# Kernel optimization log

Measured on AMD Instinct MI355X. Metric: run time of the kernel, lower is better.

The kernel has to match this reference:

```python
import jax, jax.numpy as jnp
import numpy as np

# Llama config (TinyLlama-scale)
L, H, KVH, D = 2, 32, 8, 64      # layers, q heads, kv heads, head_dim
DM, FF, V = 2048, 8192, 32000    # d_model, intermediate, vocab
B, S = 1, 1024                   # batch, seq_len
EPS, THETA = 1e-5, 10000.0


def setup_inputs() -> dict:
    key = jax.random.key(0)
    ks = jax.random.split(key, 10)
    w = lambda k, shape: jax.random.normal(k, shape, jnp.float32) * 0.02
    return {
        "input_ids": jax.random.randint(ks[0], (B, S), 0, V, dtype=jnp.int32),
        "embed": w(ks[1], (V, DM)),
        "wq": w(ks[2], (L, DM, H * D)),
        "wk": w(ks[3], (L, DM, KVH * D)),
        "wv": w(ks[4], (L, DM, KVH * D)),
        "wo": w(ks[5], (L, H * D, DM)),
        "wgate": w(ks[6], (L, DM, FF)),
        "wup": w(ks[7], (L, DM, FF)),
        "wdown": w(ks[8], (L, FF, DM)),
        "ln1": jnp.ones((L, DM), jnp.float32),
        "ln2": jnp.ones((L, DM), jnp.float32),
    }


def _rms(h, g):
    return h * jax.lax.rsqrt(jnp.mean(h * h, axis=-1, keepdims=True) + EPS) * g


def _rotate_half(t):
    t1, t2 = jnp.split(t, 2, axis=-1)
    return jnp.concatenate([-t2, t1], axis=-1)


def reference(input_ids, embed, wq, wk, wv, wo, wgate, wup, wdown, ln1, ln2):
    x = embed[input_ids]                                  # (B,S,DM)
    # rotary embeddings (HF llama style)
    inv_freq = 1.0 / (THETA ** (jnp.arange(0, D, 2, dtype=jnp.float32) / D))
    freqs = jnp.arange(S, dtype=jnp.float32)[:, None] * inv_freq[None, :]
    emb = jnp.concatenate([freqs, freqs], axis=-1)        # (S,D)
    cos = jnp.cos(emb)[None, None]                        # (1,1,S,D)
    sin = jnp.sin(emb)[None, None]
    # eager causal additive mask (1,1,S,S)
    mask = jnp.triu(jnp.full((1, 1, S, S), jnp.finfo(jnp.float32).min, jnp.float32), k=1)
    scale = 1.0 / np.sqrt(D).astype(np.float32)
    for l in range(L):
        # self-attention block
        h = _rms(x, ln1[l])
        q = (h @ wq[l]).reshape(B, S, H, D).transpose(0, 2, 1, 3)     # (B,H,S,D)
        k = (h @ wk[l]).reshape(B, S, KVH, D).transpose(0, 2, 1, 3)   # (B,KVH,S,D)
        v = (h @ wv[l]).reshape(B, S, KVH, D).transpose(0, 2, 1, 3)
        q = q * cos + _rotate_half(q) * sin
        k = k * cos + _rotate_half(k) * sin
        k = jnp.repeat(k, H // KVH, axis=1)                           # GQA expand
        v = jnp.repeat(v, H // KVH, axis=1)
        scores = jnp.einsum('bhqd,bhkd->bhqk', q, k) * scale + mask   # eager path
        probs = jax.nn.softmax(scores, axis=-1)
        attn = jnp.einsum('bhqk,bhkd->bhqd', probs, v)
        attn = attn.transpose(0, 2, 1, 3).reshape(B, S, H * D)
        x = x + attn @ wo[l]
        # SwiGLU MLP block
        h = _rms(x, ln2[l])
        x = x + (jax.nn.silu(h @ wgate[l]) * (h @ wup[l])) @ wdown[l]
    return x
```

## Files before the change

kernel.cpp:

```cpp
#include <hip/hip_runtime.h>
#include <hip/hip_bf16.h>
#include <math.h>

#define NL 2
#define NH 32
#define NKVH 8
#define HD 64
#define DM 2048
#define FF 8192
#define SEQ 1024
#define QKVW 3072
#define RMS_EPS 1e-5f

typedef short s8v __attribute__((ext_vector_type(8)));
typedef short s4v __attribute__((ext_vector_type(4)));
typedef float f32x4 __attribute__((ext_vector_type(4)));
typedef __hip_bfloat16 bf16;

__global__ __launch_bounds__(256) void embed_kernel(const int* __restrict__ ids,
                                                    const float* __restrict__ emb,
                                                    float* __restrict__ x) {
    int s = blockIdx.x;
    int row = ids[s];
    const float4* src = (const float4*)(emb + (size_t)row * DM);
    float4* dst = (float4*)(x + (size_t)s * DM);
    #pragma unroll
    for (int i = 0; i < 2; ++i)
        dst[threadIdx.x + i * 256] = src[threadIdx.x + i * 256];
}

__global__ __launch_bounds__(256) void rms_kernel(const float* __restrict__ x,
                                                  const float* __restrict__ g,
                                                  bf16* __restrict__ out) {
    int s = blockIdx.x;
    const float4* row = (const float4*)(x + (size_t)s * DM);
    float4 v0 = row[threadIdx.x * 2];
    float4 v1 = row[threadIdx.x * 2 + 1];
    float ss = v0.x*v0.x + v0.y*v0.y + v0.z*v0.z + v0.w*v0.w
             + v1.x*v1.x + v1.y*v1.y + v1.z*v1.z + v1.w*v1.w;
    #pragma unroll
    for (int o = 32; o > 0; o >>= 1) ss += __shfl_down(ss, o, 64);
    __shared__ float red[4];
    if ((threadIdx.x & 63) == 0) red[threadIdx.x >> 6] = ss;
    __syncthreads();
    float total = red[0] + red[1] + red[2] + red[3];
    float inv = 1.0f / sqrtf(total / (float)DM + RMS_EPS);
    const float4* g4 = (const float4*)g;
    float4 ga = g4[threadIdx.x * 2], gb = g4[threadIdx.x * 2 + 1];
    union { bf16 h[8]; s8v v; } u;
    u.h[0] = __float2bfloat16(v0.x * inv * ga.x);
    u.h[1] = __float2bfloat16(v0.y * inv * ga.y);
    u.h[2] = __float2bfloat16(v0.z * inv * ga.z);
    u.h[3] = __float2bfloat16(v0.w * inv * ga.w);
    u.h[4] = __float2bfloat16(v1.x * inv * gb.x);
    u.h[5] = __float2bfloat16(v1.y * inv * gb.y);
    u.h[6] = __float2bfloat16(v1.z * inv * gb.z);
    u.h[7] = __float2bfloat16(v1.w * inv * gb.w);
    *(s8v*)(out + (size_t)s * DM + threadIdx.x * 8) = u.v;
}

template<bool OUTBF>
__global__ __launch_bounds__(256) void gemm_f32w_kernel(const bf16* __restrict__ A, int Ka,
                                                        const float* __restrict__ Wa, int Na,
                                                        const float* __restrict__ Wb, int Nb,
                                                        const float* __restrict__ Wc,
                                                        float* __restrict__ C,
                                                        bf16* __restrict__ Cb,
                                                        int M, int N, int Kchunk) {
    __shared__ bf16 As[2][128 * 64];
    __shared__ bf16 Bs[2][128 * 64];
    const int t = threadIdx.x, lane = t & 63;
    const int w = t >> 6;
    const int m0 = blockIdx.y * 128, n0 = blockIdx.x * 128;
    const size_t koff = (size_t)blockIdx.z * Kchunk;

    const int nl = t & 127;
    const int kob = t >> 7;
    const int ng = n0 + nl;
    const float* wp; int wstr;
    if (ng < Na)           { wp = Wa + ng;             wstr = Na; }
    else if (ng < Na + Nb) { wp = Wb + (ng - Na);      wstr = Nb; }
    else                   { wp = Wc + (ng - Na - Nb); wstr = N - Na - Nb; }
    wp += koff * (size_t)wstr;

    const int ako = t & 7, am = t >> 3;
    const bf16* apt = A + (size_t)(m0 + am) * Ka + koff + ako * 8;

    const int wm = (w >> 1) * 64, wn = (w & 1) * 64;
    const int fr = lane & 15, sl = lane >> 4;

    f32x4 acc[4][4];
    f32x4 z = {0.f, 0.f, 0.f, 0.f};
    #pragma unroll
    for (int i = 0; i < 4; ++i)
        #pragma unroll
        for (int j = 0; j < 4; ++j) acc[i][j] = z;

    float rb[4][8];
    s8v ra[4];

    auto LOADR = [&](int tile) {
        const int k0 = tile * 64;
        #pragma unroll
        for (int u = 0; u < 4; ++u) {
            const float* p = wp + (size_t)(k0 + (kob + 2 * u) * 8) * wstr;
            #pragma unroll
            for (int j = 0; j < 8; ++j) rb[u][j] = p[(size_t)j * wstr];
            ra[u] = *(const s8v*)(apt + (size_t)(32 * u) * Ka + k0);
        }
    };
    auto WRITE = [&](bf16* AsB, bf16* BsB) {
        #pragma unroll
        for (int u = 0; u < 4; ++u) {
            union { bf16 h[8]; s8v v; } cv;
            #pragma unroll
            for (int j = 0; j < 8; ++j) cv.h[j] = __float2bfloat16(rb[u][j]);
            int ko = kob + 2 * u;
            *(s8v*)((char*)BsB + nl * 128 + ((ko * 16) ^ ((nl & 7) << 4))) = cv.v;
            int m = am + 32 * u;
            *(s8v*)((char*)AsB + m * 128 + ((ako * 16) ^ ((m & 7) << 4))) = ra[u];
        }
    };
    auto COMPUTE = [&](const bf16* AsB, const bf16* BsB) {
        #pragma unroll
        for (int kk = 0; kk < 2; ++kk) {
            const int kb = kk * 64 + sl * 16;
            s8v af[4], bfv[4];
            #pragma unroll
            for (int i = 0; i < 4; ++i) {
                int m = wm + i * 16 + fr;
                af[i] = *(const s8v*)((const char*)AsB + m * 128 + (kb ^ ((m & 7) << 4)));
            }
            #pragma unroll
            for (int j = 0; j < 4; ++j) {
                int n = wn + j * 16 + fr;
                bfv[j] = *(const s8v*)((const char*)BsB + n * 128 + (kb ^ ((n & 7) << 4)));
            }
            #pragma unroll
            for (int i = 0; i < 4; ++i)
                #pragma unroll
                for (int j = 0; j < 4; ++j)
                    acc[i][j] = __builtin_amdgcn_mfma_f32_16x16x32_bf16(af[i], bfv[j], acc[i][j], 0, 0, 0);
        }
    };

    const int nt = Kchunk / 64;
    LOADR(0);
    WRITE(&As[0][0], &Bs[0][0]);
    __syncthreads();
    for (int tt = 0; tt < nt; ++tt) {
        const int cur = tt & 1;
        if (tt + 1 < nt) LOADR(tt + 1);
        COMPUTE(&As[cur][0], &Bs[cur][0]);
        if (tt + 1 < nt) {
            __syncthreads();
            WRITE(&As[cur ^ 1][0], &Bs[cur ^ 1][0]);
            __syncthreads();
        }
    }

    float* Cz = C + (size_t)blockIdx.z * M * N;
    #pragma unroll
    for (int i = 0; i < 4; ++i) {
        #pragma unroll
        for (int j = 0; j < 4; ++j) {
            #pragma unroll
            for (int q = 0; q < 4; ++q) {
                int row = m0 + wm + i * 16 + sl * 4 + q;
                int col = n0 + wn + j * 16 + fr;
                float vv = acc[i][j][q];
                if constexpr (OUTBF) Cb[(size_t)row * N + col] = __float2bfloat16(vv);
                else                 Cz[(size_t)row * N + col] = vv;
            }
        }
    }
}

__global__ __launch_bounds__(512) void gemm256_kernel(const bf16* __restrict__ A, int Ka,
                                                      const float* __restrict__ Wa, int Na,
                                                      const float* __restrict__ Wb,
                                                      bf16* __restrict__ Cb,
                                                      int M, int N, int K) {
    __shared__ bf16 As[2][256 * 64];
    __shared__ bf16 Bs[2][256 * 64];
    const int t = threadIdx.x, lane = t & 63;
    const int w = t >> 6;
    const int m0 = blockIdx.y * 256, n0 = blockIdx.x * 256;

    const int nl = t & 255;
    const int kob = t >> 8;
    const int ng = n0 + nl;
    const float* wp; int wstr;
    if (ng < Na) { wp = Wa + ng;        wstr = Na; }
    else         { wp = Wb + (ng - Na); wstr = N - Na; }

    const int ako = t & 7, am = t >> 3;
    const bf16* apt = A + (size_t)(m0 + am) * Ka + ako * 8;

    const int wm = (w >> 2) * 128, wn = (w & 3) * 64;
    const int fr = lane & 15, sl = lane >> 4;

    f32x4 acc[8][4];
    f32x4 z = {0.f, 0.f, 0.f, 0.f};
    #pragma unroll
    for (int i = 0; i < 8; ++i)
        #pragma unroll
        for (int j = 0; j < 4; ++j) acc[i][j] = z;

    float rb[4][8];
    s8v ra[4];

    auto LOADR = [&](int tile) {
        const int k0 = tile * 64;
        #pragma unroll
        for (int u = 0; u < 4; ++u) {
            const float* p = wp + (size_t)(k0 + (kob + 2 * u) * 8) * wstr;
            #pragma unroll
            for (int j = 0; j < 8; ++j) rb[u][j] = p[(size_t)j * wstr];
            ra[u] = *(const s8v*)(apt + (size_t)(64 * u) * Ka + k0);
        }
    };
    auto WRITE = [&](bf16* AsB, bf16* BsB) {
        #pragma unroll
        for (int u = 0; u < 4; ++u) {
            union { bf16 h[8]; s8v v; } cv;
            #pragma unroll
            for (int j = 0; j < 8; ++j) cv.h[j] = __float2bfloat16(rb[u][j]);
            int ko = kob + 2 * u;
            *(s8v*)((char*)BsB + nl * 128 + ((ko * 16) ^ ((nl & 7) << 4))) = cv.v;
            int m = am + 64 * u;
            *(s8v*)((char*)AsB + m * 128 + ((ako * 16) ^ ((m & 7) << 4))) = ra[u];
        }
    };
    auto COMPUTE = [&](const bf16* AsB, const bf16* BsB) {
        #pragma unroll
        for (int kk = 0; kk < 2; ++kk) {
            const int kb = kk * 64 + sl * 16;
            s8v af[8], bfv[4];
            #pragma unroll
            for (int i = 0; i < 8; ++i) {
                int m = wm + i * 16 + fr;
                af[i] = *(const s8v*)((const char*)AsB + m * 128 + (kb ^ ((m & 7) << 4)));
            }
            #pragma unroll
            for (int j = 0; j < 4; ++j) {
                int n = wn + j * 16 + fr;
                bfv[j] = *(const s8v*)((const char*)BsB + n * 128 + (kb ^ ((n & 7) << 4)));
            }
            #pragma unroll
            for (int i = 0; i < 8; ++i)
                #pragma unroll
                for (int j = 0; j < 4; ++j)
                    acc[i][j] = __builtin_amdgcn_mfma_f32_16x16x32_bf16(af[i], bfv[j], acc[i][j], 0, 0, 0);
        }
    };

    const int nt = K / 64;
    LOADR(0);
    WRITE(&As[0][0], &Bs[0][0]);
    __syncthreads();
    for (int tt = 0; tt < nt; ++tt) {
        const int cur = tt & 1;
        if (tt + 1 < nt) LOADR(tt + 1);
        COMPUTE(&As[cur][0], &Bs[cur][0]);
        if (tt + 1 < nt) {
            __syncthreads();
            WRITE(&As[cur ^ 1][0], &Bs[cur ^ 1][0]);
            __syncthreads();
        }
    }

    #pragma unroll
    for (int i = 0; i < 8; ++i) {
        #pragma unroll
        for (int j = 0; j < 4; ++j) {
            #pragma unroll
            for (int q = 0; q < 4; ++q) {
                int row = m0 + wm + i * 16 + sl * 4 + q;
                int col = n0 + wn + j * 16 + fr;
                Cb[(size_t)row * N + col] = __float2bfloat16(acc[i][j][q]);
            }
        }
    }
}

__global__ __launch_bounds__(256) void reduce4_kernel(float* __restrict__ x,
                                                      const float* __restrict__ p) {
    const int n4 = SEQ * DM / 4;
    int i = blockIdx.x * 256 + threadIdx.x;
    if (i >= n4) return;
    float4 a = ((const float4*)x)[i];
    #pragma unroll
    for (int c = 0; c < 4; ++c) {
        float4 v = ((const float4*)p)[i + c * n4];
        a.x += v.x; a.y += v.y; a.z += v.z; a.w += v.w;
    }
    ((float4*)x)[i] = a;
}

__global__ __launch_bounds__(256) void rope_qk_kernel(const float* __restrict__ qkv,
                                                      bf16* __restrict__ Qh,
                                                      bf16* __restrict__ Kh) {
    int idx = blockIdx.x * 256 + threadIdx.x;
    int i = idx & 31;
    int hh = (idx >> 5) % (NH + NKVH);
    int s = idx / (32 * (NH + NKVH));
    bool isq = hh < NH;
    int col = isq ? hh * HD + i : DM + (hh - NH) * HD + i;
    float a = qkv[(size_t)s * QKVW + col];
    float b = qkv[(size_t)s * QKVW + col + 32];
    float inv = exp2f(-(float)i * 0.41524101186092029f);
    float ang = (float)s * inv;
    float c = cosf(ang), sn = sinf(ang);
    float ra = a * c - b * sn;
    float rb = b * c + a * sn;
    if (isq) {
        bf16* p = Qh + ((size_t)hh * SEQ + s) * HD + i;
        p[0]  = __float2bfloat16(ra);
        p[32] = __float2bfloat16(rb);
    } else {
        bf16* p = Kh + ((size_t)(hh - NH) * SEQ + s) * HD + i;
        p[0]  = __float2bfloat16(ra);
        p[32] = __float2bfloat16(rb);
    }
}

__global__ __launch_bounds__(256) void vtrans_kernel(const float* __restrict__ qkv,
                                                     bf16* __restrict__ Vt) {
    __shared__ float tile[64][65];
    const int s0 = blockIdx.x * 64;
    const int kvh = blockIdx.y;
    const int tx = threadIdx.x & 63, ty = threadIdx.x >> 6;
    #pragma unroll
    for (int i = 0; i < 16; ++i)
        tile[i * 4 + ty][tx] = qkv[(size_t)(s0 + i * 4 + ty) * QKVW + DM + 512 + kvh * HD + tx];
    __syncthreads();
    #pragma unroll
    for (int i = 0; i < 16; ++i) {
        int d = i * 4 + ty;
        Vt[((size_t)kvh * HD + d) * SEQ + s0 + tx] = __float2bfloat16(tile[tx][d]);
    }
}

__global__ __launch_bounds__(256) void attn_mfma_kernel(const bf16* __restrict__ Qh,
                                                        const bf16* __restrict__ Kh,
                                                        const bf16* __restrict__ Vt,
                                                        bf16* __restrict__ o) {
    __shared__ char lds[32768];
    char* Qs = lds;
    char* Ks = lds + 8192;
    char* Vs = lds + 16384;
    char* Ps = lds + 24576;
    const int t = threadIdx.x, lane = t & 63, w = t >> 6;
    const int g = lane >> 4, lo = lane & 15;
    const int h = blockIdx.y, kvh = h >> 2;
    const int qbase = blockIdx.x * 64;
    const int strip = w * 16;
    const bf16* qsrc = Qh + ((size_t)h * SEQ + qbase) * HD;
    const bf16* ksrc = Kh + (size_t)kvh * SEQ * HD;
    const bf16* vsrc = Vt + (size_t)kvh * HD * SEQ;

    #pragma unroll
    for (int c = t; c < 512; c += 256) {
        int row = c >> 3, col = c & 7;
        *(s8v*)(Qs + row * 128 + ((col * 16) ^ ((row & 7) << 4))) =
            *(const s8v*)(qsrc + row * HD + col * 8);
    }

    f32x4 oacc[4];
    f32x4 z = {0.f, 0.f, 0.f, 0.f};
    #pragma unroll
    for (int dj = 0; dj < 4; ++dj) oacc[dj] = z;
    float m0[4], lsum[4];
    #pragma unroll
    for (int r = 0; r < 4; ++r) { m0[r] = -INFINITY; lsum[r] = 0.f; }

    const int qt = blockIdx.x;
    for (int kt = 0; kt <= qt; ++kt) {
        __syncthreads();
        const bf16* kq = ksrc + (size_t)(kt * 64) * HD;
        const bf16* vq = vsrc + kt * 64;
        #pragma unroll
        for (int c = t; c < 512; c += 256) {
            int row = c >> 3, col = c & 7;
            int swz = (col * 16) ^ ((row & 7) << 4);
            *(s8v*)(Ks + row * 128 + swz) = *(const s8v*)(kq + row * HD + col * 8);
            *(s8v*)(Vs + row * 128 + swz) = *(const s8v*)(vq + (size_t)row * SEQ + col * 8);
        }
        __syncthreads();

        s8v qa0 = *(const s8v*)(Qs + (strip + lo) * 128 + ((g * 16) ^ ((lo & 7) << 4)));
        s8v qa1 = *(const s8v*)(Qs + (strip + lo) * 128 + ((64 + g * 16) ^ ((lo & 7) << 4)));
        f32x4 sacc[4];
        #pragma unroll
        for (int j = 0; j < 4; ++j) {
            s8v kb0 = *(const s8v*)(Ks + (j * 16 + lo) * 128 + ((g * 16) ^ ((lo & 7) << 4)));
            s8v kb1 = *(const s8v*)(Ks + (j * 16 + lo) * 128 + ((64 + g * 16) ^ ((lo & 7) << 4)));
            f32x4 sv = __builtin_amdgcn_mfma_f32_16x16x32_bf16(qa0, kb0, z, 0, 0, 0);
            sacc[j] = __builtin_amdgcn_mfma_f32_16x16x32_bf16(qa1, kb1, sv, 0, 0, 0);
        }
        #pragma unroll
        for (int j = 0; j < 4; ++j) {
            int kgl = kt * 64 + j * 16 + lo;
            #pragma unroll
            for (int r = 0; r < 4; ++r) {
                int qgl = qbase + strip + g * 4 + r;
                float sv = sacc[j][r] * 0.125f;
                sacc[j][r] = (kgl <= qgl) ? sv : -INFINITY;
            }
        }
        float rmax[4], resc[4];
        #pragma unroll
        for (int r = 0; r < 4; ++r) {
            float mx = fmaxf(fmaxf(sacc[0][r], sacc[1][r]), fmaxf(sacc[2][r], sacc[3][r]));
            mx = fmaxf(mx, __shfl_xor(mx, 1, 64));
            mx = fmaxf(mx, __shfl_xor(mx, 2, 64));
            mx = fmaxf(mx, __shfl_xor(mx, 4, 64));
            mx = fmaxf(mx, __shfl_xor(mx, 8, 64));
            float mn = fmaxf(m0[r], mx);
            resc[r] = expf(m0[r] - mn);
            m0[r] = mn;
            rmax[r] = mn;
        }
        #pragma unroll
        for (int j = 0; j < 4; ++j)
            #pragma unroll
            for (int r = 0; r < 4; ++r)
                sacc[j][r] = expf(sacc[j][r] - rmax[r]);
        #pragma unroll
        for (int r = 0; r < 4; ++r) {
            float ps = sacc[0][r] + sacc[1][r] + sacc[2][r] + sacc[3][r];
            lsum[r] = lsum[r] * resc[r] + ps;
        }
        #pragma unroll
        for (int dj = 0; dj < 4; ++dj)
            #pragma unroll
            for (int r = 0; r < 4; ++r)
                oacc[dj][r] *= resc[r];
        #pragma unroll
        for (int j = 0; j < 4; ++j) {
            #pragma unroll
            for (int r = 0; r < 4; ++r) {
                int prow = strip + g * 4 + r;
                int pcol = j * 16 + lo;
                *(bf16*)(Ps + prow * 128 + ((pcol * 2) ^ ((prow & 7) << 4))) =
                    __float2bfloat16(sacc[j][r]);
            }
        }
        s8v pa0 = *(const s8v*)(Ps + (strip + lo) * 128 + ((g * 16) ^ ((lo & 7) << 4)));
        s8v pa1 = *(const s8v*)(Ps + (strip + lo) * 128 + ((64 + g * 16) ^ ((lo & 7) << 4)));
        #pragma unroll
        for (int dj = 0; dj < 4; ++dj) {
            s8v vb0 = *(const s8v*)(Vs + (dj * 16 + lo) * 128 + ((g * 16) ^ ((lo & 7) << 4)));
            s8v vb1 = *(const s8v*)(Vs + (dj * 16 + lo) * 128 + ((64 + g * 16) ^ ((lo & 7) << 4)));
            oacc[dj] = __builtin_amdgcn_mfma_f32_16x16x32_bf16(pa0, vb0, oacc[dj], 0, 0, 0);
            oacc[dj] = __builtin_amdgcn_mfma_f32_16x16x32_bf16(pa1, vb1, oacc[dj], 0, 0, 0);
        }
    }
    float invl[4];
    #pragma unroll
    for (int r = 0; r < 4; ++r) {
        float l = lsum[r];
        l += __shfl_xor(l, 1, 64);
        l += __shfl_xor(l, 2, 64);
        l += __shfl_xor(l, 4, 64);
        l += __shfl_xor(l, 8, 64);
        invl[r] = 1.f / l;
    }
    #pragma unroll
    for (int dj = 0; dj < 4; ++dj) {
        #pragma unroll
        for (int r = 0; r < 4; ++r) {
            int qrow = qbase + strip + g * 4 + r;
            o[(size_t)qrow * DM + h * HD + dj * 16 + lo] =
                __float2bfloat16(oacc[dj][r] * invl[r]);
        }
    }
}

__global__ __launch_bounds__(256) void silu_mul_kernel(const bf16* __restrict__ gu,
                                                       bf16* __restrict__ ga) {
    int i = blockIdx.x * 256 + threadIdx.x;
    int s = i >> 10;
    int c8 = i & 1023;
    union { s8v v; bf16 h[8]; } gv, uv, ov;
    gv.v = *(const s8v*)(gu + (size_t)s * (2 * FF) + c8 * 8);
    uv.v = *(const s8v*)(gu + (size_t)s * (2 * FF) + FF + c8 * 8);
    #pragma unroll
    for (int j = 0; j < 8; ++j) {
        float g = __bfloat162float(gv.h[j]);
        float u = __bfloat162float(uv.h[j]);
        ov.h[j] = __float2bfloat16(g / (1.f + expf(-g)) * u);
    }
    *(s8v*)(ga + (size_t)s * FF + c8 * 8) = ov.v;
}

extern "C" void kernel_launch(void* const* d_in, const int* in_sizes, int n_in,
                              void* d_out, int out_size, void* d_ws, size_t ws_size,
                              hipStream_t stream) {
    const int*   ids   = (const int*)d_in[0];
    const float* emb   = (const float*)d_in[1];
    const float* wq    = (const float*)d_in[2];
    const float* wk    = (const float*)d_in[3];
    const float* wv    = (const float*)d_in[4];
    const float* wo    = (const float*)d_in[5];
    const float* wgate = (const float*)d_in[6];
    const float* wup   = (const float*)d_in[7];
    const float* wdown = (const float*)d_in[8];
    const float* ln1   = (const float*)d_in[9];
    const float* ln2   = (const float*)d_in[10];
    float* x = (float*)d_out;

    bf16* h_bf  = (bf16*)d_ws;
    bf16* attnb = h_bf  + (size_t)SEQ * DM;
    bf16* gub   = attnb + (size_t)SEQ * DM;
    bf16* gab   = gub   + (size_t)SEQ * 2 * FF;
    bf16* Qhb   = gab   + (size_t)SEQ * FF;
    bf16* Khb   = Qhb   + (size_t)NH * SEQ * HD;
    bf16* Vtb   = Khb   + (size_t)NKVH * SEQ * HD;
    float* qkv  = (float*)(Vtb + (size_t)NKVH * HD * SEQ);
    float* psum = qkv + (size_t)SEQ * QKVW;

    embed_kernel<<<SEQ, 256, 0, stream>>>(ids, emb, x);

    for (int l = 0; l < NL; ++l) {
        const float* wq_l = wq + (size_t)l * DM * DM;
        const float* wk_l = wk + (size_t)l * DM * 512;
        const float* wv_l = wv + (size_t)l * DM * 512;
        const float* wo_l = wo + (size_t)l * DM * DM;
        const float* wg_l = wgate + (size_t)l * DM * FF;
        const float* wu_l = wup   + (size_t)l * DM * FF;
        const float* wd_l = wdown + (size_t)l * FF * DM;

        rms_kernel<<<SEQ, 256, 0, stream>>>(x, ln1 + (size_t)l * DM, h_bf);

        gemm_f32w_kernel<false><<<dim3(QKVW / 128, SEQ / 128, 1), 256, 0, stream>>>(
            h_bf, DM, wq_l, DM, wk_l, 512, wv_l, qkv, nullptr, SEQ, QKVW, DM);

        rope_qk_kernel<<<(SEQ * (NH + NKVH) * 32) / 256, 256, 0, stream>>>(qkv, Qhb, Khb);
        vtrans_kernel<<<dim3(SEQ / 64, NKVH), 256, 0, stream>>>(qkv, Vtb);

        attn_mfma_kernel<<<dim3(SEQ / 64, NH), 256, 0, stream>>>(Qhb, Khb, Vtb, attnb);

        gemm_f32w_kernel<false><<<dim3(DM / 128, SEQ / 128, 4), 256, 0, stream>>>(
            attnb, DM, wo_l, DM, nullptr, 0, nullptr, psum, nullptr, SEQ, DM, DM / 4);
        reduce4_kernel<<<(SEQ * DM / 4) / 256, 256, 0, stream>>>(x, psum);

        rms_kernel<<<SEQ, 256, 0, stream>>>(x, ln2 + (size_t)l * DM, h_bf);

        gemm256_kernel<<<dim3((2 * FF) / 256, SEQ / 256), 512, 0, stream>>>(
            h_bf, DM, wg_l, FF, wu_l, gub, SEQ, 2 * FF, DM);

        silu_mul_kernel<<<(SEQ * FF / 8) / 256, 256, 0, stream>>>(gub, gab);

        gemm_f32w_kernel<false><<<dim3(DM / 128, SEQ / 128, 4), 256, 0, stream>>>(
            gab, FF, wd_l, DM, nullptr, 0, nullptr, psum, nullptr, SEQ, DM, FF / 4);
        reduce4_kernel<<<(SEQ * DM / 4) / 256, 256, 0, stream>>>(x, psum);
    }
}
```

Baseline: 624.2 us.

## Fuse RoPE and V-transpose into QKV GEMM epilogue; fuse SiLU-mul into gate/up GEMM

A dedicated QKV GEMM now applies rotary embedding to Q/K and writes transposed bf16 V directly from registers, which drops the fp32 qkv buffer and the rope and vtrans kernels. The gate/up GEMM interleaves matching gate and up column tiles per block, passes the up half through LDS and applies SiLU*up in the epilogue, which drops the intermediate gu buffer and the silu kernel. The aim is to save launches and global round trips. The cost is scattered bf16 stores and cos/sin evaluation in the epilogue, plus a 128KB LDS footprint in the gate/up kernel.

After: 722.3 us. +15.7%, slower.

```diff
diff --git a/kernel.cpp b/kernel.cpp
--- a/kernel.cpp
+++ b/kernel.cpp
@@ -59,13 +59,9 @@
     *(s8v*)(out + (size_t)s * DM + threadIdx.x * 8) = u.v;
 }
 
-template<bool OUTBF>
 __global__ __launch_bounds__(256) void gemm_f32w_kernel(const bf16* __restrict__ A, int Ka,
                                                         const float* __restrict__ Wa, int Na,
-                                                        const float* __restrict__ Wb, int Nb,
-                                                        const float* __restrict__ Wc,
                                                         float* __restrict__ C,
-                                                        bf16* __restrict__ Cb,
                                                         int M, int N, int Kchunk) {
     __shared__ bf16 As[2][128 * 64];
     __shared__ bf16 Bs[2][128 * 64];
@@ -76,12 +72,8 @@
 
     const int nl = t & 127;
     const int kob = t >> 7;
-    const int ng = n0 + nl;
-    const float* wp; int wstr;
-    if (ng < Na)           { wp = Wa + ng;             wstr = Na; }
-    else if (ng < Na + Nb) { wp = Wb + (ng - Na);      wstr = Nb; }
-    else                   { wp = Wc + (ng - Na - Nb); wstr = N - Na - Nb; }
-    wp += koff * (size_t)wstr;
+    const float* wp = Wa + n0 + nl + koff * (size_t)Na;
+    const int wstr = Na;
 
     const int ako = t & 7, am = t >> 3;
     const bf16* apt = A + (size_t)(m0 + am) * Ka + koff + ako * 8;
@@ -168,42 +160,43 @@
             for (int q = 0; q < 4; ++q) {
                 int row = m0 + wm + i * 16 + sl * 4 + q;
                 int col = n0 + wn + j * 16 + fr;
-                float vv = acc[i][j][q];
-                if constexpr (OUTBF) Cb[(size_t)row * N + col] = __float2bfloat16(vv);
-                else                 Cz[(size_t)row * N + col] = vv;
-            }
-        }
-    }
-}
-
-__global__ __launch_bounds__(512) void gemm256_kernel(const bf16* __restrict__ A, int Ka,
-                                                      const float* __restrict__ Wa, int Na,
-                                                      const float* __restrict__ Wb,
-                                                      bf16* __restrict__ Cb,
-                                                      int M, int N, int K) {
-    __shared__ bf16 As[2][256 * 64];
-    __shared__ bf16 Bs[2][256 * 64];
+                Cz[(size_t)row * N + col] = acc[i][j][q];
+            }
+        }
+    }
+}
+
+__global__ __launch_bounds__(256) void gemm_qkv_kernel(const bf16* __restrict__ A,
+                                                       const float* __restrict__ Wq,
+                                                       const float* __restrict__ Wk,
+                                                       const float* __restrict__ Wv,
+                                                       bf16* __restrict__ Qh,
+                                                       bf16* __restrict__ Kh,
+                                                       bf16* __restrict__ Vt) {
+    __shared__ bf16 As[2][128 * 64];
+    __shared__ bf16 Bs[2][128 * 64];
     const int t = threadIdx.x, lane = t & 63;
     const int w = t >> 6;
-    const int m0 = blockIdx.y * 256, n0 = blockIdx.x * 256;
-
-    const int nl = t & 255;
-    const int kob = t >> 8;
+    const int m0 = blockIdx.y * 128, n0 = blockIdx.x * 128;
+
+    const int nl = t & 127;
+    const int kob = t >> 7;
     const int ng = n0 + nl;
     const float* wp; int wstr;
-    if (ng < Na) { wp = Wa + ng;        wstr = Na; }
-    else         { wp = Wb + (ng - Na); wstr = N - Na; }
+    if (ng < DM)            { wp = Wq + ng;          wstr = DM;  }
+    else if (ng < DM + 512) { wp = Wk + (ng - DM);   wstr = 512; }
+    else                    { wp = Wv + (ng - 2560); wstr = 512; }
 
     const int ako = t & 7, am = t >> 3;
-    const bf16* apt = A + (size_t)(m0 + am) * Ka + ako * 8;
-
-    const int wm = (w >> 2) * 128, wn = (w & 3) * 64;
+    const bf16* apt = A + (size_t)(m0 + am) * DM + ako * 8;
+
+    const int wm = (w >> 1) * 64, wn = (w & 1) * 64;
     const int fr = lane & 15, sl = lane >> 4;
 
-    f32x4 acc[8][4];
+    f32x4 acc[4][4];
     f32x4 z = {0.f, 0.f, 0.f, 0.f};
     #pragma unroll
-    for (int i = 0; i < 8; ++i)
+    for (int i = 0; i < 4; ++i)
         #pragma unroll
         for (int j = 0; j < 4; ++j) acc[i][j] = z;
 
@@ -217,7 +210,7 @@
             const float* p = wp + (size_t)(k0 + (kob + 2 * u) * 8) * wstr;
             #pragma unroll
             for (int j = 0; j < 8; ++j) rb[u][j] = p[(size_t)j * wstr];
-            ra[u] = *(const s8v*)(apt + (size_t)(64 * u) * Ka + k0);
+            ra[u] = *(const s8v*)(apt + (size_t)(32 * u) * DM + k0);
         }
     };
     auto WRITE = [&](bf16* AsB, bf16* BsB) {
@@ -228,7 +221,7 @@
             for (int j = 0; j < 8; ++j) cv.h[j] = __float2bfloat16(rb[u][j]);
             int ko = kob + 2 * u;
             *(s8v*)((char*)BsB + nl * 128 + ((ko * 16) ^ ((nl & 7) << 4))) = cv.v;
-            int m = am + 64 * u;
+            int m = am + 32 * u;
             *(s8v*)((char*)AsB + m * 128 + ((ako * 16) ^ ((m & 7) << 4))) = ra[u];
         }
     };
@@ -236,9 +229,9 @@
         #pragma unroll
         for (int kk = 0; kk < 2; ++kk) {
             const int kb = kk * 64 + sl * 16;
-            s8v af[8], bfv[4];
-            #pragma unroll
-            for (int i = 0; i < 8; ++i) {
+            s8v af[4], bfv[4];
+            #pragma unroll
+            for (int i = 0; i < 4; ++i) {
                 int m = wm + i * 16 + fr;
                 af[i] = *(const s8v*)((const char*)AsB + m * 128 + (kb ^ ((m & 7) << 4)));
             }
@@ -248,14 +241,14 @@
                 bfv[j] = *(const s8v*)((const char*)BsB + n * 128 + (kb ^ ((n & 7) << 4)));
             }
             #pragma unroll
-            for (int i = 0; i < 8; ++i)
+            for (int i = 0; i < 4; ++i)
                 #pragma unroll
                 for (int j = 0; j < 4; ++j)
                     acc[i][j] = __builtin_amdgcn_mfma_f32_16x16x32_bf16(af[i], bfv[j], acc[i][j], 0, 0, 0);
         }
     };
 
-    const int nt = K / 64;
+    const int nt = DM / 64;
     LOADR(0);
     WRITE(&As[0][0], &Bs[0][0]);
     __syncthreads();
@@ -271,14 +264,165 @@
     }
 
     #pragma unroll
-    for (int i = 0; i < 8; ++i) {
-        #pragma unroll
-        for (int j = 0; j < 4; ++j) {
-            #pragma unroll
-            for (int q = 0; q < 4; ++q) {
-                int row = m0 + wm + i * 16 + sl * 4 + q;
-                int col = n0 + wn + j * 16 + fr;
-                Cb[(size_t)row * N + col] = __float2bfloat16(acc[i][j][q]);
+    for (int j = 0; j < 4; ++j) {
+        int c = n0 + wn + j * 16 + fr;
+        if (c < 2560) {
+            if (j < 2) {
+                int ii = (wn + j * 16 + fr) & 63;
+                bf16* dst = (c < DM) ? Qh + ((size_t)(c >> 6) * SEQ) * HD
+                                     : Kh + ((size_t)((c - DM) >> 6) * SEQ) * HD;
+                float invf = exp2f(-(float)ii * 0.41524101186092029f);
+                #pragma unroll
+                for (int i = 0; i < 4; ++i) {
+                    #pragma unroll
+                    for (int q = 0; q < 4; ++q) {
+                        int s = m0 + wm + i * 16 + sl * 4 + q;
+                        float a = acc[i][j][q], b = acc[i][j + 2][q];
+                        float ang = (float)s * invf;
+                        float cs = cosf(ang), sn = sinf(ang);
+                        bf16* p = dst + (size_t)s * HD + ii;
+                        p[0]  = __float2bfloat16(a * cs - b * sn);
+                        p[32] = __float2bfloat16(b * cs + a * sn);
+                    }
+                }
+            }
+        } else {
+            int kvh = (c - 2560) >> 6, d = (c - 2560) & 63;
+            bf16* dst = Vt + ((size_t)kvh * HD + d) * SEQ;
+            #pragma unroll
+            for (int i = 0; i < 4; ++i) {
+                #pragma unroll
+                for (int q = 0; q < 4; ++q) {
+                    int s = m0 + wm + i * 16 + sl * 4 + q;
+                    dst[s] = __float2bfloat16(acc[i][j][q]);
+                }
+            }
+        }
+    }
+}
+
+__global__ __launch_bounds__(512) void gemm_gu_kernel(const bf16* __restrict__ A,
+                                                      const float* __restrict__ Wg,
+                                                      const float* __restrict__ Wu,
+                                                      bf16* __restrict__ gab) {
+    __shared__ char lds[131072];
+    const int t = threadIdx.x, lane = t & 63;
+    const int w = t >> 6;
+    const int m0 = blockIdx.y * 256, n0g = blockIdx.x * 128;
+
+    const int nl = t & 255;
+    const int kob = t >> 8;
+    const int cl = nl & 127;
+    const float* wp = ((nl < 128) ? Wg : Wu) + n0g + cl;
+    const int wstr = FF;
+
+    const int ako = t & 7, am = t >> 3;
+    const bf16* apt = A + (size_t)(m0 + am) * DM + ako * 8;
+
+    const int wm = (w >> 2) * 128, wn = (w & 3) * 64;
+    const int fr = lane & 15, sl = lane >> 4;
+
+    f32x4 acc[8][4];
+    f32x4 z = {0.f, 0.f, 0.f, 0.f};
+    #pragma unroll
+    for (int i = 0; i < 8; ++i)
+        #pragma unroll
+        for (int j = 0; j < 4; ++j) acc[i][j] = z;
+
+    float rb[4][8];
+    s8v ra[4];
+
+    auto LOADR = [&](int tile) {
+        const int k0 = tile * 64;
+        #pragma unroll
+        for (int u = 0; u < 4; ++u) {
+            const float* p = wp + (size_t)(k0 + (kob + 2 * u) * 8) * wstr;
+            #pragma unroll
+            for (int j = 0; j < 8; ++j) rb[u][j] = p[(size_t)j * wstr];
+            ra[u] = *(const s8v*)(apt + (size_t)(64 * u) * DM + k0);
+        }
+    };
+    auto WRITE = [&](char* AsB, char* BsB) {
+        #pragma unroll
+        for (int u = 0; u < 4; ++u) {
+            union { bf16 h[8]; s8v v; } cv;
+            #pragma unroll
+            for (int j = 0; j < 8; ++j) cv.h[j] = __float2bfloat16(rb[u][j]);
+            int ko = kob + 2 * u;
+            *(s8v*)(BsB + nl * 128 + ((ko * 16) ^ ((nl & 7) << 4))) = cv.v;
+            int m = am + 64 * u;
+            *(s8v*)(AsB + m * 128 + ((ako * 16) ^ ((m & 7) << 4))) = ra[u];
+        }
+    };
+    auto COMPUTE = [&](const char* AsB, const char* BsB) {
+        #pragma unroll
+        for (int kk = 0; kk < 2; ++kk) {
+            const int kb = kk * 64 + sl * 16;
+            s8v af[8], bfv[4];
+            #pragma unroll
+            for (int i = 0; i < 8; ++i) {
+                int m = wm + i * 16 + fr;
+                af[i] = *(const s8v*)(AsB + m * 128 + (kb ^ ((m & 7) << 4)));
+            }
+            #pragma unroll
+            for (int j = 0; j < 4; ++j) {
+                int n = wn + j * 16 + fr;
+                bfv[j] = *(const s8v*)(BsB + n * 128 + (kb ^ ((n & 7) << 4)));
+            }
+            #pragma unroll
+            for (int i = 0; i < 8; ++i)
+                #pragma unroll
+                for (int j = 0; j < 4; ++j)
+                    acc[i][j] = __builtin_amdgcn_mfma_f32_16x16x32_bf16(af[i], bfv[j], acc[i][j], 0, 0, 0);
+        }
+    };
+
+    const int nt = DM / 64;
+    LOADR(0);
+    WRITE(lds, lds + 65536);
+    __syncthreads();
+    for (int tt = 0; tt < nt; ++tt) {
+        const int cur = tt & 1;
+        if (tt + 1 < nt) LOADR(tt + 1);
+        COMPUTE(lds + cur * 32768, lds + 65536 + cur * 32768);
+        if (tt + 1 < nt) {
+            __syncthreads();
+            WRITE(lds + (cur ^ 1) * 32768, lds + 65536 + (cur ^ 1) * 32768);
+            __syncthreads();
+        }
+    }
+
+    __syncthreads();
+    bf16* Ups = (bf16*)lds;
+    if (wn >= 128) {
+        #pragma unroll
+        for (int i = 0; i < 8; ++i) {
+            #pragma unroll
+            for (int j = 0; j < 4; ++j) {
+                #pragma unroll
+                for (int q = 0; q < 4; ++q) {
+                    int row = wm + i * 16 + sl * 4 + q;
+                    int col = (wn - 128) + j * 16 + fr;
+                    Ups[row * 130 + col] = __float2bfloat16(acc[i][j][q]);
+                }
+            }
+        }
+    }
+    __syncthreads();
+    if (wn < 128) {
+        #pragma unroll
+        for (int i = 0; i < 8; ++i) {
+            #pragma unroll
+            for (int j = 0; j < 4; ++j) {
+                #pragma unroll
+                for (int q = 0; q < 4; ++q) {
+                    int row = wm + i * 16 + sl * 4 + q;
+                    int col = wn + j * 16 + fr;
+                    float g = acc[i][j][q];
+                    float u = __bfloat162float(Ups[row * 130 + col]);
+                    gab[(size_t)(m0 + row) * FF + n0g + col] =
+                        __float2bfloat16(g / (1.f + expf(-g)) * u);
+                }
             }
         }
     }
@@ -296,50 +440,6 @@
         a.x += v.x; a.y += v.y; a.z += v.z; a.w += v.w;
     }
     ((float4*)x)[i] = a;
-}
-
-__global__ __launch_bounds__(256) void rope_qk_kernel(const float* __restrict__ qkv,
-                                                      bf16* __restrict__ Qh,
-                                                      bf16* __restrict__ Kh) {
-    int idx = blockIdx.x * 256 + threadIdx.x;
-    int i = idx & 31;
-    int hh = (idx >> 5) % (NH + NKVH);
-    int s = idx / (32 * (NH + NKVH));
-    bool isq = hh < NH;
-    int col = isq ? hh * HD + i : DM + (hh - NH) * HD + i;
-    float a = qkv[(size_t)s * QKVW + col];
-    float b = qkv[(size_t)s * QKVW + col + 32];
-    float inv = exp2f(-(float)i * 0.41524101186092029f);
-    float ang = (float)s * inv;
-    float c = cosf(ang), sn = sinf(ang);
-    float ra = a * c - b * sn;
-    float rb = b * c + a * sn;
-    if (isq) {
-        bf16* p = Qh + ((size_t)hh * SEQ + s) * HD + i;
-        p[0]  = __float2bfloat16(ra);
-        p[32] = __float2bfloat16(rb);
-    } else {
-        bf16* p = Kh + ((size_t)(hh - NH) * SEQ + s) * HD + i;
-        p[0]  = __float2bfloat16(ra);
-        p[32] = __float2bfloat16(rb);
-    }
-}
-
-__global__ __launch_bounds__(256) void vtrans_kernel(const float* __restrict__ qkv,
-                                                     bf16* __restrict__ Vt) {
-    __shared__ float tile[64][65];
-    const int s0 = blockIdx.x * 64;
-    const int kvh = blockIdx.y;
-    const int tx = threadIdx.x & 63, ty = threadIdx.x >> 6;
-    #pragma unroll
-    for (int i = 0; i < 16; ++i)
-        tile[i * 4 + ty][tx] = qkv[(size_t)(s0 + i * 4 + ty) * QKVW + DM + 512 + kvh * HD + tx];
-    __syncthreads();
-    #pragma unroll
-    for (int i = 0; i < 16; ++i) {
-        int d = i * 4 + ty;
-        Vt[((size_t)kvh * HD + d) * SEQ + s0 + tx] = __float2bfloat16(tile[tx][d]);
-    }
 }
 
 __global__ __launch_bounds__(256) void attn_mfma_kernel(const bf16* __restrict__ Qh,
@@ -478,23 +578,6 @@
     }
 }
 
-__global__ __launch_bounds__(256) void silu_mul_kernel(const bf16* __restrict__ gu,
-                                                       bf16* __restrict__ ga) {
-    int i = blockIdx.x * 256 + threadIdx.x;
-    int s = i >> 10;
-    int c8 = i & 1023;
-    union { s8v v; bf16 h[8]; } gv, uv, ov;
-    gv.v = *(const s8v*)(gu + (size_t)s * (2 * FF) + c8 * 8);
-    uv.v = *(const s8v*)(gu + (size_t)s * (2 * FF) + FF + c8 * 8);
-    #pragma unroll
-    for (int j = 0; j < 8; ++j) {
-        float g = __bfloat162float(gv.h[j]);
-        float u = __bfloat162float(uv.h[j]);
-        ov.h[j] = __float2bfloat16(g / (1.f + expf(-g)) * u);
-    }
-    *(s8v*)(ga + (size_t)s * FF + c8 * 8) = ov.v;
-}
-
 extern "C" void kernel_launch(void* const* d_in, const int* in_sizes, int n_in,
                               void* d_out, int out_size, void* d_ws, size_t ws_size,
                               hipStream_t stream) {
@@ -513,13 +596,11 @@
 
     bf16* h_bf  = (bf16*)d_ws;
     bf16* attnb = h_bf  + (size_t)SEQ * DM;
-    bf16* gub   = attnb + (size_t)SEQ * DM;
-    bf16* gab   = gub   + (size_t)SEQ * 2 * FF;
+    bf16* gab   = attnb + (size_t)SEQ * DM;
     bf16* Qhb   = gab   + (size_t)SEQ * FF;
     bf16* Khb   = Qhb   + (size_t)NH * SEQ * HD;
     bf16* Vtb   = Khb   + (size_t)NKVH * SEQ * HD;
-    float* qkv  = (float*)(Vtb + (size_t)NKVH * HD * SEQ);
-    float* psum = qkv + (size_t)SEQ * QKVW;
+    float* psum = (float*)(Vtb + (size_t)NKVH * HD * SEQ);
 
     embed_kernel<<<SEQ, 256, 0, stream>>>(ids, emb, x);
 
@@ -534,27 +615,22 @@
 
         rms_kernel<<<SEQ, 256, 0, stream>>>(x, ln1 + (size_t)l * DM, h_bf);
 
-        gemm_f32w_kernel<false><<<dim3(QKVW / 128, SEQ / 128, 1), 256, 0, stream>>>(
-            h_bf, DM, wq_l, DM, wk_l, 512, wv_l, qkv, nullptr, SEQ, QKVW, DM);
-
-        rope_qk_kernel<<<(SEQ * (NH + NKVH) * 32) / 256, 256, 0, stream>>>(qkv, Qhb, Khb);
-        vtrans_kernel<<<dim3(SEQ / 64, NKVH), 256, 0, stream>>>(qkv, Vtb);
+        gemm_qkv_kernel<<<dim3(QKVW / 128, SEQ / 128), 256, 0, stream>>>(
+            h_bf, wq_l, wk_l, wv_l, Qhb, Khb, Vtb);
 
         attn_mfma_kernel<<<dim3(SEQ / 64, NH), 256, 0, stream>>>(Qhb, Khb, Vtb, attnb);
 
-        gemm_f32w_kernel<false><<<dim3(DM / 128, SEQ / 128, 4), 256, 0, stream>>>(
-            attnb, DM, wo_l, DM, nullptr, 0, nullptr, psum, nullptr, SEQ, DM, DM / 4);
+        gemm_f32w_kernel<<<dim3(DM / 128, SEQ / 128, 4), 256, 0, stream>>>(
+            attnb, DM, wo_l, DM, psum, SEQ, DM, DM / 4);
         reduce4_kernel<<<(SEQ * DM / 4) / 256, 256, 0, stream>>>(x, psum);
 
         rms_kernel<<<SEQ, 256, 0, stream>>>(x, ln2 + (size_t)l * DM, h_bf);
 
-        gemm256_kernel<<<dim3((2 * FF) / 256, SEQ / 256), 512, 0, stream>>>(
-            h_bf, DM, wg_l, FF, wu_l, gub, SEQ, 2 * FF, DM);
-
-        silu_mul_kernel<<<(SEQ * FF / 8) / 256, 256, 0, stream>>>(gub, gab);
-
-        gemm_f32w_kernel<false><<<dim3(DM / 128, SEQ / 128, 4), 256, 0, stream>>>(
-            gab, FF, wd_l, DM, nullptr, 0, nullptr, psum, nullptr, SEQ, DM, FF / 4);
+        gemm_gu_kernel<<<dim3(FF / 128, SEQ / 256), 512, 0, stream>>>(
+            h_bf, wg_l, wu_l, gab);
+
+        gemm_f32w_kernel<<<dim3(DM / 128, SEQ / 128, 4), 256, 0, stream>>>(
+            gab, FF, wd_l, DM, psum, SEQ, DM, FF / 4);
         reduce4_kernel<<<(SEQ * DM / 4) / 256, 256, 0, stream>>>(x, psum);
     }
 }
```

## Prefetch fp32 weight tiles two iterations ahead in GEMM main loop

Applied to the files above, without the earlier changes.

Splits the global load of the fp32 weight (B) tile from the bf16 activation (A) tile and double-buffers the weight registers (rbA/rbB). The weight load is now issued two k-tiles ahead, while the activation load stays one tile ahead, and the loop is unrolled by two with fixed LDS buffer indices. The aim is to hide the latency of the strided, uncoalesced fp32 weight reads behind more MFMA work. It doubles the weight staging registers, which may cut occupancy or cause spills.

Result: slower. 727.0 us (+16.5%).

```diff
diff --git a/kernel.cpp b/kernel.cpp
--- a/kernel.cpp
+++ b/kernel.cpp
@@ -96,20 +96,25 @@
         #pragma unroll
         for (int j = 0; j < 4; ++j) acc[i][j] = z;
 
-    float rb[4][8];
+    float rbA[4][8], rbB[4][8];
     s8v ra[4];
 
-    auto LOADR = [&](int tile) {
+    auto LOADB = [&](float (&rb)[4][8], int tile) {
         const int k0 = tile * 64;
         #pragma unroll
         for (int u = 0; u < 4; ++u) {
             const float* p = wp + (size_t)(k0 + (kob + 2 * u) * 8) * wstr;
             #pragma unroll
             for (int j = 0; j < 8; ++j) rb[u][j] = p[(size_t)j * wstr];
+        }
+    };
+    auto LOADA = [&](int tile) {
+        const int k0 = tile * 64;
+        #pragma unroll
+        for (int u = 0; u < 4; ++u)
             ra[u] = *(const s8v*)(apt + (size_t)(32 * u) * Ka + k0);
-        }
-    };
-    auto WRITE = [&](bf16* AsB, bf16* BsB) {
+    };
+    auto WRITE = [&](bf16* AsB, bf16* BsB, float (&rb)[4][8]) {
         #pragma unroll
         for (int u = 0; u < 4; ++u) {
             union { bf16 h[8]; s8v v; } cv;
@@ -145,17 +150,26 @@
     };
 
     const int nt = Kchunk / 64;
-    LOADR(0);
-    WRITE(&As[0][0], &Bs[0][0]);
+    LOADB(rbA, 0); LOADA(0);
+    WRITE(&As[0][0], &Bs[0][0], rbA);
+    if (nt > 1) LOADB(rbA, 1);
     __syncthreads();
-    for (int tt = 0; tt < nt; ++tt) {
-        const int cur = tt & 1;
-        if (tt + 1 < nt) LOADR(tt + 1);
-        COMPUTE(&As[cur][0], &Bs[cur][0]);
+    for (int tt = 0; tt < nt; tt += 2) {
+        if (tt + 2 < nt) LOADB(rbB, tt + 2);
+        if (tt + 1 < nt) LOADA(tt + 1);
+        COMPUTE(&As[0][0], &Bs[0][0]);
         if (tt + 1 < nt) {
             __syncthreads();
-            WRITE(&As[cur ^ 1][0], &Bs[cur ^ 1][0]);
+            WRITE(&As[1][0], &Bs[1][0], rbA);
             __syncthreads();
+            if (tt + 3 < nt) LOADB(rbA, tt + 3);
+            if (tt + 2 < nt) LOADA(tt + 2);
+            COMPUTE(&As[1][0], &Bs[1][0]);
+            if (tt + 2 < nt) {
+                __syncthreads();
+                WRITE(&As[0][0], &Bs[0][0], rbB);
+                __syncthreads();
+            }
         }
     }
 
```
